# Kernel tuning notes

Hardware: AMD Instinct MI355X
Metric: run time of the kernel (lower is better)

The kernel has to match this reference:

```python
import jax, jax.numpy as jnp
import numpy as np

B, N, DIM = 2, 8192, 3
K = 16            # num_neighbours (dilation=1)
R = 2048          # num_representitives
CIN, CL, COUT = 64, 16, 128
K2 = K * K


def _bn(x, g, b):
    # BatchNorm in eval mode with running_mean=0, running_var=1 -> affine
    return x * g + b


def setup_inputs() -> dict:
    key = jax.random.key(0)
    ks = jax.random.split(key, 24)
    r = lambda i, shape, s=1.0: jax.random.normal(ks[i], shape, jnp.float32) * s
    return {
        "points": r(0, (B, N, DIM)),
        "features": r(1, (B, N, CIN)),
        "lift_w": r(2, (CL, DIM), 0.3), "lift_b": r(3, (CL,), 0.1),
        "bn_lift_g": 1.0 + r(4, (CL,), 0.1), "bn_lift_b": r(5, (CL,), 0.1),
        "t1_w": r(6, (K2, DIM * K), 0.1), "t1_b": r(7, (K2,), 0.1),
        "bn1_g": 1.0 + r(8, (K2,), 0.1), "bn1_b": r(9, (K2,), 0.1),
        "t2_w": r(10, (K2, K2), 0.05), "t2_b": r(11, (K2,), 0.1),
        "bn2_g": 1.0 + r(12, (K2,), 0.1), "bn2_b": r(13, (K2,), 0.1),
        "t3_w": r(14, (K2, K2), 0.05), "t3_b": r(15, (K2,), 0.1),
        "bn3_g": 1.0 + r(16, (K2,), 0.1), "bn3_b": r(17, (K2,), 0.1),
        "conv_w": r(18, (COUT, CIN + CL, K), 0.05), "conv_b": r(19, (COUT,), 0.1),
        "rep_idx": jax.random.permutation(ks[20], N)[:R],
    }


def reference(points, features, lift_w, lift_b, bn_lift_g, bn_lift_b,
              t1_w, t1_b, bn1_g, bn1_b, t2_w, t2_b, bn2_g, bn2_b,
              t3_w, t3_b, bn3_g, bn3_b, conv_w, conv_b, rep_idx):
    b, n, _ = points.shape
    # ---- KNN (squared distance is order-equivalent to torch.cdist) ----
    sq = jnp.sum(points * points, -1)                                   # (b,n)
    d2 = sq[:, :, None] + sq[:, None, :] - 2.0 * jnp.einsum('bnd,bmd->bnm', points, points)
    _, idx = jax.lax.top_k(-d2, K + 1)                                  # (b,n,K+1)
    nn_idx = idx[:, :, 1:]                                              # drop self
    # ---- representative sampling + neighbor gather ----
    rep_pos = points[:, rep_idx]                                        # (b,R,3)
    nb_idx = nn_idx[:, rep_idx]                                         # (b,R,K)
    gather = jax.vmap(lambda arr, i: arr[i])
    nbr_pos = gather(points, nb_idx)                                    # (b,R,K,3)
    nbr_feat = gather(features, nb_idx)                                 # (b,R,K,CIN)
    # ---- X_conv ----
    p = (nbr_pos - rep_pos[:, :, None, :]).reshape(b * R, K, DIM)       # centered
    lifted = jax.nn.relu(_bn(p @ lift_w.T + lift_b, bn_lift_g, bn_lift_b))  # (bR,K,CL)
    feat = jnp.concatenate([lifted, nbr_feat.reshape(b * R, K, CIN)], -1)   # (bR,K,CL+CIN)
    pf = p.reshape(b * R, K * DIM)
    h = jax.nn.relu(_bn(pf @ t1_w.T + t1_b, bn1_g, bn1_b))
    h = jax.nn.relu(_bn(h @ t2_w.T + t2_b, bn2_g, bn2_b))
    T = _bn(h @ t3_w.T + t3_b, bn3_g, bn3_b).reshape(b * R, K, K)       # learned transform
    Tf = jnp.einsum('bij,bjc->bic', T, feat)                            # bmm, (bR,K,C)
    # Conv1d(C, COUT, kernel=K) over length K -> single output position
    out = jnp.einsum('bkc,ock->bo', Tf, conv_w) + conv_b                # (bR,COUT)
    return rep_pos, out.reshape(b, R, COUT)
```

## Files before the change

### kernel.cpp

```cpp
#include <hip/hip_runtime.h>
#include <float.h>

#define Bn 2
#define Nn 8192
#define Rr 2048
#define Kk 16
#define CIN 64
#define CL 16
#define COUT 128
#define K2c 256
#define GT (Bn*Rr)
#define FD (CL+CIN)
#define KC (Kk*FD)
#define MG 4

__global__ __launch_bounds__(256) void prep_kernel(
    const float* __restrict__ t1_w, const float* __restrict__ t2_w,
    const float* __restrict__ t3_w, const float* __restrict__ conv_w,
    const float* __restrict__ points,
    float* __restrict__ t1t, float* __restrict__ t2t,
    float* __restrict__ t3t, float* __restrict__ wp,
    float4* __restrict__ pts4)
{
  int i = blockIdx.x * 256 + threadIdx.x;
  if (i < K2c*48) { int j = i / 48, k = i - j*48; t1t[k*K2c + j] = t1_w[i]; }
  if (i < K2c*K2c) { int j = i >> 8, k = i & 255; t2t[k*K2c + j] = t2_w[i]; t3t[k*K2c + j] = t3_w[i]; }
  if (i < COUT*KC) {
    int o = i / KC, ck = i - o*KC;
    int c = ck >> 4, k = ck & 15;
    wp[(k*FD + c)*COUT + o] = conv_w[i];
  }
  if (i < Bn*Nn) {
    float x = points[i*3+0], y = points[i*3+1], z = points[i*3+2];
    float sq = __fadd_rn(__fadd_rn(__fmul_rn(x,x), __fmul_rn(y,y)), __fmul_rn(z,z));
    pts4[i] = make_float4(x, y, z, sq);
  }
}

__global__ __launch_bounds__(512) void knn_kernel(
    const float4* __restrict__ pts4, const int* __restrict__ rep_idx,
    int* __restrict__ nb_idx, float* __restrict__ p_out,
    float* __restrict__ rep_pos_out)
{
  __shared__ float4 ptsS[3072];
  __shared__ unsigned long long coll[8][128];
  int t    = threadIdx.x;
  int lane = t & 63;
  int w    = t >> 6;
  int g    = blockIdx.x * 8 + w;
  int b    = g >> 11;
  int r    = g & 2047;
  int n    = rep_idx[r];
  const float4* pb4 = pts4 + (size_t)b*Nn;
  float4 Q = pb4[n];
  float qx = Q.x, qy = Q.y, qz = Q.z, sqn = Q.w;

  float c0 = FLT_MAX, c1 = FLT_MAX, c2 = FLT_MAX;
  for (int c = 0; c < 3; c++) {
    int base  = c * 3072;
    int count = (c < 2) ? 3072 : 2048;
    __syncthreads();
    for (int i = t; i < count; i += 512) ptsS[i] = pb4[base + i];
    __syncthreads();
    int iters = count >> 6;
    #pragma unroll 4
    for (int j = 0; j < iters; j++) {
      float4 P = ptsS[j*64 + lane];
      float dot = __fmaf_rn(qz, P.z, __fmaf_rn(qy, P.y, __fmul_rn(qx, P.x)));
      float d2  = __fsub_rn(__fadd_rn(sqn, P.w), __fmul_rn(2.0f, dot));
      float nc2 = __builtin_amdgcn_fmed3f(c1, c2, d2);
      float nc1 = __builtin_amdgcn_fmed3f(c0, c1, d2);
      float nc0 = fminf(c0, d2);
      c0 = nc0; c1 = nc1; c2 = nc2;
    }
  }

  float tau = FLT_MAX;
  for (int rnd = 0; rnd < 6; rnd++) {
    float m = c2;
    #pragma unroll
    for (int off = 1; off < 64; off <<= 1) m = fminf(m, __shfl_xor(m, off));
    if (c2 == m) c2 = FLT_MAX;
    tau = m;
  }

  int cnt = 0;
  #pragma unroll
  for (int cc = 0; cc < 3; cc++) {
    int c = (cc == 0) ? 2 : (cc - 1);
    int base  = c * 3072;
    int count = (c < 2) ? 3072 : 2048;
    if (cc != 0) {
      __syncthreads();
      for (int i = t; i < count; i += 512) ptsS[i] = pb4[base + i];
      __syncthreads();
    }
    int iters = count >> 6;
    #pragma unroll 4
    for (int j = 0; j < iters; j++) {
      float4 P = ptsS[j*64 + lane];
      float dot = __fmaf_rn(qz, P.z, __fmaf_rn(qy, P.y, __fmul_rn(qx, P.x)));
      float d2  = __fsub_rn(__fadd_rn(sqn, P.w), __fmul_rn(2.0f, dot));
      bool pr = (d2 <= tau);
      unsigned long long mask = __ballot(pr);
      if (pr) {
        int pos = cnt + (int)__popcll(mask & ((1ull << lane) - 1ull));
        if (pos < 128) {
          unsigned f = __float_as_uint(d2);
          unsigned mono = f ^ ((unsigned)((int)f >> 31) | 0x80000000u);
          coll[w][pos] = ((unsigned long long)mono << 32) | (unsigned)(base + j*64 + lane);
        }
      }
      cnt += (int)__popcll(mask);
    }
  }
  if (cnt > 128) cnt = 128;

  unsigned long long e1 = (lane < cnt)      ? coll[w][lane]      : ~0ull;
  unsigned long long e2 = (lane + 64 < cnt) ? coll[w][lane + 64] : ~0ull;
  int out_m = 0;
  for (int rnd = 0; rnd < 17; rnd++) {
    unsigned long long myk = (e1 < e2) ? e1 : e2;
    unsigned long long kmin = myk;
    #pragma unroll
    for (int off = 1; off < 64; off <<= 1) {
      unsigned long long o = __shfl_xor(kmin, off);
      kmin = (o < kmin) ? o : kmin;
    }
    if (rnd >= 1 && lane == rnd - 1) out_m = (int)(kmin & 0xFFFFFFFFull);
    if (kmin == e1) e1 = ~0ull;
    else if (kmin == e2) e2 = ~0ull;
  }

  if (lane < 16) {
    nb_idx[g*Kk + lane] = out_m;
    float4 P = pb4[out_m];
    p_out[(g*Kk + lane)*3 + 0] = __fsub_rn(P.x, qx);
    p_out[(g*Kk + lane)*3 + 1] = __fsub_rn(P.y, qy);
    p_out[(g*Kk + lane)*3 + 2] = __fsub_rn(P.z, qz);
  }
  if (lane < 3) rep_pos_out[g*3 + lane] = (lane == 0 ? qx : (lane == 1 ? qy : qz));
}

__device__ __forceinline__ void fma_g(float4& a, float hv, const float4& wv) {
  a.x = fmaf(hv, wv.x, a.x);
  a.y = fmaf(hv, wv.y, a.y);
  a.z = fmaf(hv, wv.z, a.z);
  a.w = fmaf(hv, wv.w, a.w);
}

__global__ __launch_bounds__(256) void mlp_kernel(
    const float* __restrict__ p,
    const float* __restrict__ t1t, const float* __restrict__ t1_b,
    const float* __restrict__ g1v, const float* __restrict__ b1v,
    const float* __restrict__ t2t, const float* __restrict__ t2_b,
    const float* __restrict__ g2v, const float* __restrict__ b2v,
    const float* __restrict__ t3t, const float* __restrict__ t3_b,
    const float* __restrict__ g3v, const float* __restrict__ b3v,
    float* __restrict__ T_out)
{
  __shared__ float pf[48][MG];
  __shared__ float hA[K2c][MG];
  __shared__ float red[4*16*66];
  int t = threadIdx.x;
  int w = t >> 6, l = t & 63;
  int g0 = blockIdx.x * MG;
  for (int e = t; e < MG*48; e += 256) {
    int g = e / 48, k = e - g*48;
    pf[k][g] = p[(size_t)(g0+g)*48 + k];
  }
  __syncthreads();

  float4 acc[MG];

#define LDW(WSRC, K) (*(const float4*)&WSRC[(size_t)(K)*K2c + 4*l])

#define KSTAGE(WSRC, KDIM, HBUF, WB, KK, KNEXT)                        \
  {                                                                    \
    float4 wc = WB;                                                    \
    if ((KNEXT) < KDIM) WB = LDW(WSRC, KNEXT);                         \
    float4 h = *(const float4*)&HBUF[KK][0];                           \
    fma_g(acc[0], h.x, wc); fma_g(acc[1], h.y, wc);                    \
    fma_g(acc[2], h.z, wc); fma_g(acc[3], h.w, wc);                    \
  }

#define KLOOP(WSRC, KDIM, HBUF)                                        \
  {                                                                    \
    _Pragma("unroll")                                                  \
    for (int q = 0; q < MG; q++) acc[q] = make_float4(0.f,0.f,0.f,0.f);\
    float4 wb0 = LDW(WSRC, w);                                         \
    float4 wb1 = (w + 4  < KDIM) ? LDW(WSRC, w + 4)  : wb0;            \
    float4 wb2 = (w + 8  < KDIM) ? LDW(WSRC, w + 8)  : wb0;            \
    float4 wb3 = (w + 12 < KDIM) ? LDW(WSRC, w + 12) : wb0;            \
    for (int k = w; k < KDIM; k += 16) {                               \
      KSTAGE(WSRC, KDIM, HBUF, wb0, k,      k + 16)                    \
      if (k + 4 < KDIM)  KSTAGE(WSRC, KDIM, HBUF, wb1, k + 4,  k + 20) \
      if (k + 8 < KDIM)  KSTAGE(WSRC, KDIM, HBUF, wb2, k + 8,  k + 24) \
      if (k + 12 < KDIM) KSTAGE(WSRC, KDIM, HBUF, wb3, k + 12, k + 28) \
    }                                                                  \
  }

#define WRITE_RED()                                                    \
  {                                                                    \
    _Pragma("unroll")                                                  \
    for (int q = 0; q < MG; q++) {                                     \
      red[(w*16 + 0*4 + q)*66 + l] = acc[q].x;                         \
      red[(w*16 + 1*4 + q)*66 + l] = acc[q].y;                         \
      red[(w*16 + 2*4 + q)*66 + l] = acc[q].z;                         \
      red[(w*16 + 3*4 + q)*66 + l] = acc[q].w;                         \
    }                                                                  \
  }

#define REDUCE(S)                                                      \
  float4 S = make_float4(0.f,0.f,0.f,0.f);                             \
  {                                                                    \
    int lr = t >> 2, cc = t & 3;                                       \
    _Pragma("unroll")                                                  \
    for (int ww = 0; ww < 4; ww++) {                                   \
      S.x += red[(ww*16 + cc*4 + 0)*66 + lr];                          \
      S.y += red[(ww*16 + cc*4 + 1)*66 + lr];                          \
      S.z += red[(ww*16 + cc*4 + 2)*66 + lr];                          \
      S.w += red[(ww*16 + cc*4 + 3)*66 + lr];                          \
    }                                                                  \
  }

  KLOOP(t1t, 48, pf)
  WRITE_RED()
  __syncthreads();
  {
    REDUCE(s)
    float bb = t1_b[t], gg = g1v[t], oo = b1v[t];
    float4 v;
    v.x = fmaxf(fmaf(s.x + bb, gg, oo), 0.f);
    v.y = fmaxf(fmaf(s.y + bb, gg, oo), 0.f);
    v.z = fmaxf(fmaf(s.z + bb, gg, oo), 0.f);
    v.w = fmaxf(fmaf(s.w + bb, gg, oo), 0.f);
    *(float4*)&hA[t][0] = v;
  }
  __syncthreads();

  KLOOP(t2t, K2c, hA)
  WRITE_RED()
  __syncthreads();
  {
    REDUCE(s)
    float bb = t2_b[t], gg = g2v[t], oo = b2v[t];
    float4 v;
    v.x = fmaxf(fmaf(s.x + bb, gg, oo), 0.f);
    v.y = fmaxf(fmaf(s.y + bb, gg, oo), 0.f);
    v.z = fmaxf(fmaf(s.z + bb, gg, oo), 0.f);
    v.w = fmaxf(fmaf(s.w + bb, gg, oo), 0.f);
    *(float4*)&hA[t][0] = v;
  }
  __syncthreads();

  KLOOP(t3t, K2c, hA)
  WRITE_RED()
  __syncthreads();
  {
    REDUCE(s)
    float bb = t3_b[t], gg = g3v[t], oo = b3v[t];
    T_out[(size_t)(g0+0)*K2c + t] = fmaf(s.x + bb, gg, oo);
    T_out[(size_t)(g0+1)*K2c + t] = fmaf(s.y + bb, gg, oo);
    T_out[(size_t)(g0+2)*K2c + t] = fmaf(s.z + bb, gg, oo);
    T_out[(size_t)(g0+3)*K2c + t] = fmaf(s.w + bb, gg, oo);
  }
#undef KLOOP
#undef KSTAGE
#undef LDW
#undef WRITE_RED
#undef REDUCE
}

__global__ __launch_bounds__(256) void tf_kernel(
    const float* __restrict__ T_in, const float* __restrict__ features,
    const float* __restrict__ p, const int* __restrict__ nb_idx,
    const float* __restrict__ lift_w, const float* __restrict__ lift_b,
    const float* __restrict__ bng, const float* __restrict__ bnb,
    float* __restrict__ Tf)
{
  __shared__ float T_s[4*K2c];
  __shared__ float f_s[4*KC];
  __shared__ float ps[4*48];
  __shared__ int   idxs[64];
  __shared__ float lw[48], lb2[16], lg[16], lo[16];
  int t = threadIdx.x;
  int g0 = blockIdx.x * 4;
  int b = g0 / Rr;
  for (int e = t; e < 4*K2c; e += 256) T_s[e] = T_in[(size_t)g0*K2c + e];
  if (t >= 32 && t < 224) {
    int e = t - 32;
    ps[e] = p[(size_t)g0*48 + e];
  }
  if (t < 64) idxs[t] = nb_idx[g0*16 + t];
  if (t >= 64 && t < 112)  lw[t-64]   = lift_w[t-64];
  if (t >= 112 && t < 128) lb2[t-112] = lift_b[t-112];
  if (t >= 224 && t < 240) lg[t-224]  = bng[t-224];
  if (t >= 240)            lo[t-240]  = bnb[t-240];
  __syncthreads();

  {
    int wv = t >> 6, ln = t & 63;
    for (int row = wv; row < 64; row += 4) {
      int gg = row >> 4, k = row & 15;
      f_s[gg*KC + k*FD + CL + ln] = features[((size_t)b*Nn + idxs[row])*CIN + ln];
    }
  }
  for (int e = t; e < 1024; e += 256) {
    int gg = e >> 8, rem = e & 255, k = rem >> 4, c = rem & 15;
    float acc = ps[gg*48 + k*3 + 0]*lw[c*3+0] + ps[gg*48 + k*3 + 1]*lw[c*3+1]
              + ps[gg*48 + k*3 + 2]*lw[c*3+2] + lb2[c];
    acc = acc*lg[c] + lo[c];
    f_s[gg*KC + k*FD + c] = fmaxf(acc, 0.f);
  }
  __syncthreads();

  int gg = t >> 6;
  int cl = t & 63;
  for (int ci = cl; ci < FD; ci += 64) {
    float fcol[16];
    #pragma unroll
    for (int j = 0; j < 16; j++) fcol[j] = f_s[gg*KC + j*FD + ci];
    #pragma unroll
    for (int k = 0; k < 16; k++) {
      float acc = 0.f;
      #pragma unroll
      for (int j = 0; j < 16; j++) acc = fmaf(T_s[gg*K2c + k*16 + j], fcol[j], acc);
      Tf[(size_t)(g0+gg)*KC + k*FD + ci] = acc;
    }
  }
}

__global__ __launch_bounds__(256) void gemm_kernel(
    const float* __restrict__ A,
    const float* __restrict__ Bm,
    float* __restrict__ part)
{
  __shared__ float As[16*36];
  __shared__ float Bs[16*COUT];
  int t = threadIdx.x;
  int m0 = blockIdx.x * 32;
  int ky = blockIdx.y;
  int kbase0 = ky * (KC/8);
  float acc[4][4];
  #pragma unroll
  for (int i = 0; i < 4; i++)
    #pragma unroll
    for (int j = 0; j < 4; j++) acc[i][j] = 0.f;
  int tn = t & 31, tm = t >> 5;

  for (int kt = 0; kt < KC/8; kt += 16) {
    int kb = kbase0 + kt;
    {
      int kcol = t & 15, row = t >> 4;
      As[kcol*36 + row]      = A[(size_t)(m0+row)*KC + kb + kcol];
      As[kcol*36 + row + 16] = A[(size_t)(m0+row+16)*KC + kb + kcol];
    }
    {
      int o = t & 127, kk2 = t >> 7;
      #pragma unroll
      for (int p4 = 0; p4 < 8; p4++) {
        int kk = kk2 + p4*2;
        Bs[kk*COUT + o] = Bm[(size_t)(kb+kk)*COUT + o];
      }
    }
    __syncthreads();
    #pragma unroll
    for (int kk = 0; kk < 16; kk++) {
      float4 a4 = *(const float4*)&As[kk*36 + tm*4];
      float4 b4 = *(const float4*)&Bs[kk*COUT + tn*4];
      float av[4] = {a4.x, a4.y, a4.z, a4.w};
      float bv[4] = {b4.x, b4.y, b4.z, b4.w};
      #pragma unroll
      for (int i = 0; i < 4; i++)
        #pragma unroll
        for (int j = 0; j < 4; j++) acc[i][j] = fmaf(av[i], bv[j], acc[i][j]);
    }
    __syncthreads();
  }
  #pragma unroll
  for (int i = 0; i < 4; i++) {
    float4 v = make_float4(acc[i][0], acc[i][1], acc[i][2], acc[i][3]);
    *(float4*)&part[((size_t)ky*GT + m0 + tm*4 + i)*COUT + tn*4] = v;
  }
}

__global__ __launch_bounds__(256) void reduce_kernel(
    const float* __restrict__ part, const float* __restrict__ conv_b,
    float* __restrict__ outp)
{
  int i = blockIdx.x*256 + threadIdx.x;
  float4 s = ((const float4*)conv_b)[i & 31];
  #pragma unroll
  for (int w = 0; w < 8; w++) {
    float4 v = ((const float4*)(part + (size_t)w*GT*COUT))[i];
    s.x += v.x; s.y += v.y; s.z += v.z; s.w += v.w;
  }
  ((float4*)outp)[i] = s;
}

extern "C" void kernel_launch(void* const* d_in, const int* in_sizes, int n_in,
                              void* d_out, int out_size, void* d_ws, size_t ws_size,
                              hipStream_t stream) {
  const float* points   = (const float*)d_in[0];
  const float* features = (const float*)d_in[1];
  const float* lift_w   = (const float*)d_in[2];
  const float* lift_b   = (const float*)d_in[3];
  const float* bn_lift_g= (const float*)d_in[4];
  const float* bn_lift_b= (const float*)d_in[5];
  const float* t1_w     = (const float*)d_in[6];
  const float* t1_b     = (const float*)d_in[7];
  const float* bn1_g    = (const float*)d_in[8];
  const float* bn1_b    = (const float*)d_in[9];
  const float* t2_w     = (const float*)d_in[10];
  const float* t2_b     = (const float*)d_in[11];
  const float* bn2_g    = (const float*)d_in[12];
  const float* bn2_b    = (const float*)d_in[13];
  const float* t3_w     = (const float*)d_in[14];
  const float* t3_b     = (const float*)d_in[15];
  const float* bn3_g    = (const float*)d_in[16];
  const float* bn3_b    = (const float*)d_in[17];
  const float* conv_w   = (const float*)d_in[18];
  const float* conv_b   = (const float*)d_in[19];
  const int*   rep_idx  = (const int*)d_in[20];

  char* ws = (char*)d_ws;
  int*    nb   = (int*)   (ws + 0);
  float*  p    = (float*) (ws + 262144);
  float*  T    = (float*) (ws + 1048576);
  float*  Tf   = (float*) (ws + 5242880);
  float*  wp   = (float*) (ws + 26214400);
  float*  t1t  = (float*) (ws + 26869760);
  float*  t2t  = (float*) (ws + 26918912);
  float*  t3t  = (float*) (ws + 27181056);
  float*  part = (float*) (ws + 33554432);
  float4* pts4 = (float4*)(ws + 52428800);

  float* rep_pos = (float*)d_out;
  float* outp    = (float*)d_out + (size_t)GT*3;

  prep_kernel<<<640, 256, 0, stream>>>(t1_w, t2_w, t3_w, conv_w, points,
                                       t1t, t2t, t3t, wp, pts4);
  knn_kernel<<<GT/8, 512, 0, stream>>>(pts4, rep_idx, nb, p, rep_pos);
  mlp_kernel<<<GT/MG, 256, 0, stream>>>(p, t1t, t1_b, bn1_g, bn1_b,
                                        t2t, t2_b, bn2_g, bn2_b,
                                        t3t, t3_b, bn3_g, bn3_b, T);
  tf_kernel<<<GT/4, 256, 0, stream>>>(T, features, p, nb,
                                      lift_w, lift_b, bn_lift_g, bn_lift_b, Tf);
  dim3 ggrid(GT/32, 8);
  gemm_kernel<<<ggrid, 256, 0, stream>>>(Tf, wp, part);
  reduce_kernel<<<(GT*COUT/4)/256, 256, 0, stream>>>(part, conv_b, outp);
}
```

Measured before the change: 220.1 us.

## Process two queries per wave in KNN and fuse MLP with transform kernel

The KNN kernel now has each wavefront handle two representative queries, so every point loaded from shared memory serves two distance computations and the grid is halved. The MLP kernel and the feature-transform kernel are merged, so the learned 16x16 transform stays in shared memory and is no longer written to and re-read from global memory. The costs are more registers and shared memory per block, which can lower occupancy, and only 256 KNN blocks, which may underfill the GPU.

Result: slower. 277.5 us (+26.0%).

```diff
diff --git a/kernel.cpp b/kernel.cpp
--- a/kernel.cpp
+++ b/kernel.cpp
@@ -43,19 +43,21 @@
     float* __restrict__ rep_pos_out)
 {
   __shared__ float4 ptsS[3072];
-  __shared__ unsigned long long coll[8][128];
+  __shared__ unsigned long long coll[8][2][128];
   int t    = threadIdx.x;
   int lane = t & 63;
   int w    = t >> 6;
-  int g    = blockIdx.x * 8 + w;
-  int b    = g >> 11;
-  int r    = g & 2047;
-  int n    = rep_idx[r];
+  int gA   = blockIdx.x * 16 + w*2;
+  int b    = gA >> 11;
+  int rA   = gA & 2047;
+  int nA   = rep_idx[rA];
+  int nB   = rep_idx[rA + 1];
   const float4* pb4 = pts4 + (size_t)b*Nn;
-  float4 Q = pb4[n];
-  float qx = Q.x, qy = Q.y, qz = Q.z, sqn = Q.w;
-
-  float c0 = FLT_MAX, c1 = FLT_MAX, c2 = FLT_MAX;
+  float4 QA = pb4[nA];
+  float4 QB = pb4[nB];
+
+  float a0 = FLT_MAX, a1 = FLT_MAX, a2 = FLT_MAX;
+  float b0 = FLT_MAX, b1 = FLT_MAX, b2 = FLT_MAX;
   for (int c = 0; c < 3; c++) {
     int base  = c * 3072;
     int count = (c < 2) ? 3072 : 2048;
@@ -66,25 +68,38 @@
     #pragma unroll 4
     for (int j = 0; j < iters; j++) {
       float4 P = ptsS[j*64 + lane];
-      float dot = __fmaf_rn(qz, P.z, __fmaf_rn(qy, P.y, __fmul_rn(qx, P.x)));
-      float d2  = __fsub_rn(__fadd_rn(sqn, P.w), __fmul_rn(2.0f, dot));
-      float nc2 = __builtin_amdgcn_fmed3f(c1, c2, d2);
-      float nc1 = __builtin_amdgcn_fmed3f(c0, c1, d2);
-      float nc0 = fminf(c0, d2);
-      c0 = nc0; c1 = nc1; c2 = nc2;
-    }
-  }
-
-  float tau = FLT_MAX;
+      float dotA = __fmaf_rn(QA.z, P.z, __fmaf_rn(QA.y, P.y, __fmul_rn(QA.x, P.x)));
+      float d2A  = __fsub_rn(__fadd_rn(QA.w, P.w), __fmul_rn(2.0f, dotA));
+      float dotB = __fmaf_rn(QB.z, P.z, __fmaf_rn(QB.y, P.y, __fmul_rn(QB.x, P.x)));
+      float d2B  = __fsub_rn(__fadd_rn(QB.w, P.w), __fmul_rn(2.0f, dotB));
+      float na2 = __builtin_amdgcn_fmed3f(a1, a2, d2A);
+      float na1 = __builtin_amdgcn_fmed3f(a0, a1, d2A);
+      float na0 = fminf(a0, d2A);
+      a0 = na0; a1 = na1; a2 = na2;
+      float nb2 = __builtin_amdgcn_fmed3f(b1, b2, d2B);
+      float nb1 = __builtin_amdgcn_fmed3f(b0, b1, d2B);
+      float nb0 = fminf(b0, d2B);
+      b0 = nb0; b1 = nb1; b2 = nb2;
+    }
+  }
+
+  float tauA = FLT_MAX, tauB = FLT_MAX;
   for (int rnd = 0; rnd < 6; rnd++) {
-    float m = c2;
+    float m = a2;
     #pragma unroll
     for (int off = 1; off < 64; off <<= 1) m = fminf(m, __shfl_xor(m, off));
-    if (c2 == m) c2 = FLT_MAX;
-    tau = m;
-  }
-
-  int cnt = 0;
+    if (a2 == m) a2 = FLT_MAX;
+    tauA = m;
+  }
+  for (int rnd = 0; rnd < 6; rnd++) {
+    float m = b2;
+    #pragma unroll
+    for (int off = 1; off < 64; off <<= 1) m = fminf(m, __shfl_xor(m, off));
+    if (b2 == m) b2 = FLT_MAX;
+    tauB = m;
+  }
+
+  int cntA = 0, cntB = 0;
   #pragma unroll
   for (int cc = 0; cc < 3; cc++) {
     int c = (cc == 0) ? 2 : (cc - 1);
@@ -99,47 +114,69 @@
     #pragma unroll 4
     for (int j = 0; j < iters; j++) {
       float4 P = ptsS[j*64 + lane];
-      float dot = __fmaf_rn(qz, P.z, __fmaf_rn(qy, P.y, __fmul_rn(qx, P.x)));
-      float d2  = __fsub_rn(__fadd_rn(sqn, P.w), __fmul_rn(2.0f, dot));
-      bool pr = (d2 <= tau);
-      unsigned long long mask = __ballot(pr);
-      if (pr) {
-        int pos = cnt + (int)__popcll(mask & ((1ull << lane) - 1ull));
+      int m = base + j*64 + lane;
+      float dotA = __fmaf_rn(QA.z, P.z, __fmaf_rn(QA.y, P.y, __fmul_rn(QA.x, P.x)));
+      float d2A  = __fsub_rn(__fadd_rn(QA.w, P.w), __fmul_rn(2.0f, dotA));
+      bool prA = (d2A <= tauA);
+      unsigned long long maskA = __ballot(prA);
+      if (prA) {
+        int pos = cntA + (int)__popcll(maskA & ((1ull << lane) - 1ull));
         if (pos < 128) {
-          unsigned f = __float_as_uint(d2);
+          unsigned f = __float_as_uint(d2A);
           unsigned mono = f ^ ((unsigned)((int)f >> 31) | 0x80000000u);
-          coll[w][pos] = ((unsigned long long)mono << 32) | (unsigned)(base + j*64 + lane);
+          coll[w][0][pos] = ((unsigned long long)mono << 32) | (unsigned)m;
         }
       }
-      cnt += (int)__popcll(mask);
-    }
-  }
-  if (cnt > 128) cnt = 128;
-
-  unsigned long long e1 = (lane < cnt)      ? coll[w][lane]      : ~0ull;
-  unsigned long long e2 = (lane + 64 < cnt) ? coll[w][lane + 64] : ~0ull;
-  int out_m = 0;
-  for (int rnd = 0; rnd < 17; rnd++) {
-    unsigned long long myk = (e1 < e2) ? e1 : e2;
-    unsigned long long kmin = myk;
-    #pragma unroll
-    for (int off = 1; off < 64; off <<= 1) {
-      unsigned long long o = __shfl_xor(kmin, off);
-      kmin = (o < kmin) ? o : kmin;
-    }
-    if (rnd >= 1 && lane == rnd - 1) out_m = (int)(kmin & 0xFFFFFFFFull);
-    if (kmin == e1) e1 = ~0ull;
-    else if (kmin == e2) e2 = ~0ull;
-  }
-
-  if (lane < 16) {
-    nb_idx[g*Kk + lane] = out_m;
-    float4 P = pb4[out_m];
-    p_out[(g*Kk + lane)*3 + 0] = __fsub_rn(P.x, qx);
-    p_out[(g*Kk + lane)*3 + 1] = __fsub_rn(P.y, qy);
-    p_out[(g*Kk + lane)*3 + 2] = __fsub_rn(P.z, qz);
-  }
-  if (lane < 3) rep_pos_out[g*3 + lane] = (lane == 0 ? qx : (lane == 1 ? qy : qz));
+      cntA += (int)__popcll(maskA);
+      float dotB = __fmaf_rn(QB.z, P.z, __fmaf_rn(QB.y, P.y, __fmul_rn(QB.x, P.x)));
+      float d2B  = __fsub_rn(__fadd_rn(QB.w, P.w), __fmul_rn(2.0f, dotB));
+      bool prB = (d2B <= tauB);
+      unsigned long long maskB = __ballot(prB);
+      if (prB) {
+        int pos = cntB + (int)__popcll(maskB & ((1ull << lane) - 1ull));
+        if (pos < 128) {
+          unsigned f = __float_as_uint(d2B);
+          unsigned mono = f ^ ((unsigned)((int)f >> 31) | 0x80000000u);
+          coll[w][1][pos] = ((unsigned long long)mono << 32) | (unsigned)m;
+        }
+      }
+      cntB += (int)__popcll(maskB);
+    }
+  }
+  if (cntA > 128) cntA = 128;
+  if (cntB > 128) cntB = 128;
+
+  #pragma unroll
+  for (int q = 0; q < 2; q++) {
+    int cnt = q ? cntB : cntA;
+    int g   = gA + q;
+    float qx = q ? QB.x : QA.x;
+    float qy = q ? QB.y : QA.y;
+    float qz = q ? QB.z : QA.z;
+    unsigned long long e1 = (lane < cnt)      ? coll[w][q][lane]      : ~0ull;
+    unsigned long long e2 = (lane + 64 < cnt) ? coll[w][q][lane + 64] : ~0ull;
+    int out_m = 0;
+    for (int rnd = 0; rnd < 17; rnd++) {
+      unsigned long long myk = (e1 < e2) ? e1 : e2;
+      unsigned long long kmin = myk;
+      #pragma unroll
+      for (int off = 1; off < 64; off <<= 1) {
+        unsigned long long o = __shfl_xor(kmin, off);
+        kmin = (o < kmin) ? o : kmin;
+      }
+      if (rnd >= 1 && lane == rnd - 1) out_m = (int)(kmin & 0xFFFFFFFFull);
+      if (kmin == e1) e1 = ~0ull;
+      else if (kmin == e2) e2 = ~0ull;
+    }
+    if (lane < 16) {
+      nb_idx[g*Kk + lane] = out_m;
+      float4 P = pb4[out_m];
+      p_out[(g*Kk + lane)*3 + 0] = __fsub_rn(P.x, qx);
+      p_out[(g*Kk + lane)*3 + 1] = __fsub_rn(P.y, qy);
+      p_out[(g*Kk + lane)*3 + 2] = __fsub_rn(P.z, qz);
+    }
+    if (lane < 3) rep_pos_out[g*3 + lane] = (lane == 0 ? qx : (lane == 1 ? qy : qz));
+  }
 }
 
 __device__ __forceinline__ void fma_g(float4& a, float hv, const float4& wv) {
@@ -149,7 +186,7 @@
   a.w = fmaf(hv, wv.w, a.w);
 }
 
-__global__ __launch_bounds__(256) void mlp_kernel(
+__global__ __launch_bounds__(256) void mlptf_kernel(
     const float* __restrict__ p,
     const float* __restrict__ t1t, const float* __restrict__ t1_b,
     const float* __restrict__ g1v, const float* __restrict__ b1v,
@@ -157,18 +194,32 @@
     const float* __restrict__ g2v, const float* __restrict__ b2v,
     const float* __restrict__ t3t, const float* __restrict__ t3_b,
     const float* __restrict__ g3v, const float* __restrict__ b3v,
-    float* __restrict__ T_out)
+    const float* __restrict__ features, const int* __restrict__ nb_idx,
+    const float* __restrict__ lift_w, const float* __restrict__ lift_b,
+    const float* __restrict__ bng, const float* __restrict__ bnb,
+    float* __restrict__ Tf)
 {
   __shared__ float pf[48][MG];
   __shared__ float hA[K2c][MG];
-  __shared__ float red[4*16*66];
+  __shared__ float T_s[MG*K2c];
+  __shared__ float uni[MG*KC];
+  __shared__ float ps[MG*48];
+  __shared__ int   idxs[64];
+  __shared__ float lw[48], lb2[16], lg[16], lo[16];
   int t = threadIdx.x;
   int w = t >> 6, l = t & 63;
   int g0 = blockIdx.x * MG;
+  int b = g0 / Rr;
   for (int e = t; e < MG*48; e += 256) {
     int g = e / 48, k = e - g*48;
     pf[k][g] = p[(size_t)(g0+g)*48 + k];
-  }
+    ps[e]    = p[(size_t)g0*48 + e];
+  }
+  if (t < 64) idxs[t] = nb_idx[g0*16 + t];
+  if (t >= 64 && t < 112)  lw[t-64]   = lift_w[t-64];
+  if (t >= 112 && t < 128) lb2[t-112] = lift_b[t-112];
+  if (t >= 128 && t < 144) lg[t-128]  = bng[t-128];
+  if (t >= 144 && t < 160) lo[t-144]  = bnb[t-144];
   __syncthreads();
 
   float4 acc[MG];
@@ -204,10 +255,10 @@
   {                                                                    \
     _Pragma("unroll")                                                  \
     for (int q = 0; q < MG; q++) {                                     \
-      red[(w*16 + 0*4 + q)*66 + l] = acc[q].x;                         \
-      red[(w*16 + 1*4 + q)*66 + l] = acc[q].y;                         \
-      red[(w*16 + 2*4 + q)*66 + l] = acc[q].z;                         \
-      red[(w*16 + 3*4 + q)*66 + l] = acc[q].w;                         \
+      uni[(w*16 + 0*4 + q)*66 + l] = acc[q].x;                         \
+      uni[(w*16 + 1*4 + q)*66 + l] = acc[q].y;                         \
+      uni[(w*16 + 2*4 + q)*66 + l] = acc[q].z;                         \
+      uni[(w*16 + 3*4 + q)*66 + l] = acc[q].w;                         \
     }                                                                  \
   }
 
@@ -217,10 +268,10 @@
     int lr = t >> 2, cc = t & 3;                                       \
     _Pragma("unroll")                                                  \
     for (int ww = 0; ww < 4; ww++) {                                   \
-      S.x += red[(ww*16 + cc*4 + 0)*66 + lr];                          \
-      S.y += red[(ww*16 + cc*4 + 1)*66 + lr];                          \
-      S.z += red[(ww*16 + cc*4 + 2)*66 + lr];                          \
-      S.w += red[(ww*16 + cc*4 + 3)*66 + lr];                          \
+      S.x += uni[(ww*16 + cc*4 + 0)*66 + lr];                          \
+      S.y += uni[(ww*16 + cc*4 + 1)*66 + lr];                          \
+      S.z += uni[(ww*16 + cc*4 + 2)*66 + lr];                          \
+      S.w += uni[(ww*16 + cc*4 + 3)*66 + lr];                          \
     }                                                                  \
   }
 
@@ -260,75 +311,50 @@
   {
     REDUCE(s)
     float bb = t3_b[t], gg = g3v[t], oo = b3v[t];
-    T_out[(size_t)(g0+0)*K2c + t] = fmaf(s.x + bb, gg, oo);
-    T_out[(size_t)(g0+1)*K2c + t] = fmaf(s.y + bb, gg, oo);
-    T_out[(size_t)(g0+2)*K2c + t] = fmaf(s.z + bb, gg, oo);
-    T_out[(size_t)(g0+3)*K2c + t] = fmaf(s.w + bb, gg, oo);
+    T_s[0*K2c + t] = fmaf(s.x + bb, gg, oo);
+    T_s[1*K2c + t] = fmaf(s.y + bb, gg, oo);
+    T_s[2*K2c + t] = fmaf(s.z + bb, gg, oo);
+    T_s[3*K2c + t] = fmaf(s.w + bb, gg, oo);
+  }
+  __syncthreads();
+
+  {
+    int wv = t >> 6, ln = t & 63;
+    for (int row = wv; row < 64; row += 4) {
+      int gg = row >> 4, k = row & 15;
+      uni[gg*KC + k*FD + CL + ln] = features[((size_t)b*Nn + idxs[row])*CIN + ln];
+    }
+  }
+  for (int e = t; e < 1024; e += 256) {
+    int gg = e >> 8, rem = e & 255, k = rem >> 4, c = rem & 15;
+    float acc1 = ps[gg*48 + k*3 + 0]*lw[c*3+0] + ps[gg*48 + k*3 + 1]*lw[c*3+1]
+               + ps[gg*48 + k*3 + 2]*lw[c*3+2] + lb2[c];
+    acc1 = acc1*lg[c] + lo[c];
+    uni[gg*KC + k*FD + c] = fmaxf(acc1, 0.f);
+  }
+  __syncthreads();
+
+  {
+    int gg = t >> 6;
+    int cl = t & 63;
+    for (int ci = cl; ci < FD; ci += 64) {
+      float fcol[16];
+      #pragma unroll
+      for (int j = 0; j < 16; j++) fcol[j] = uni[gg*KC + j*FD + ci];
+      #pragma unroll
+      for (int k = 0; k < 16; k++) {
+        float a1 = 0.f;
+        #pragma unroll
+        for (int j = 0; j < 16; j++) a1 = fmaf(T_s[gg*K2c + k*16 + j], fcol[j], a1);
+        Tf[(size_t)(g0+gg)*KC + k*FD + ci] = a1;
+      }
+    }
   }
 #undef KLOOP
 #undef KSTAGE
 #undef LDW
 #undef WRITE_RED
 #undef REDUCE
-}
-
-__global__ __launch_bounds__(256) void tf_kernel(
-    const float* __restrict__ T_in, const float* __restrict__ features,
-    const float* __restrict__ p, const int* __restrict__ nb_idx,
-    const float* __restrict__ lift_w, const float* __restrict__ lift_b,
-    const float* __restrict__ bng, const float* __restrict__ bnb,
-    float* __restrict__ Tf)
-{
-  __shared__ float T_s[4*K2c];
-  __shared__ float f_s[4*KC];
-  __shared__ float ps[4*48];
-  __shared__ int   idxs[64];
-  __shared__ float lw[48], lb2[16], lg[16], lo[16];
-  int t = threadIdx.x;
-  int g0 = blockIdx.x * 4;
-  int b = g0 / Rr;
-  for (int e = t; e < 4*K2c; e += 256) T_s[e] = T_in[(size_t)g0*K2c + e];
-  if (t >= 32 && t < 224) {
-    int e = t - 32;
-    ps[e] = p[(size_t)g0*48 + e];
-  }
-  if (t < 64) idxs[t] = nb_idx[g0*16 + t];
-  if (t >= 64 && t < 112)  lw[t-64]   = lift_w[t-64];
-  if (t >= 112 && t < 128) lb2[t-112] = lift_b[t-112];
-  if (t >= 224 && t < 240) lg[t-224]  = bng[t-224];
-  if (t >= 240)            lo[t-240]  = bnb[t-240];
-  __syncthreads();
-
-  {
-    int wv = t >> 6, ln = t & 63;
-    for (int row = wv; row < 64; row += 4) {
-      int gg = row >> 4, k = row & 15;
-      f_s[gg*KC + k*FD + CL + ln] = features[((size_t)b*Nn + idxs[row])*CIN + ln];
-    }
-  }
-  for (int e = t; e < 1024; e += 256) {
-    int gg = e >> 8, rem = e & 255, k = rem >> 4, c = rem & 15;
-    float acc = ps[gg*48 + k*3 + 0]*lw[c*3+0] + ps[gg*48 + k*3 + 1]*lw[c*3+1]
-              + ps[gg*48 + k*3 + 2]*lw[c*3+2] + lb2[c];
-    acc = acc*lg[c] + lo[c];
-    f_s[gg*KC + k*FD + c] = fmaxf(acc, 0.f);
-  }
-  __syncthreads();
-
-  int gg = t >> 6;
-  int cl = t & 63;
-  for (int ci = cl; ci < FD; ci += 64) {
-    float fcol[16];
-    #pragma unroll
-    for (int j = 0; j < 16; j++) fcol[j] = f_s[gg*KC + j*FD + ci];
-    #pragma unroll
-    for (int k = 0; k < 16; k++) {
-      float acc = 0.f;
-      #pragma unroll
-      for (int j = 0; j < 16; j++) acc = fmaf(T_s[gg*K2c + k*16 + j], fcol[j], acc);
-      Tf[(size_t)(g0+gg)*KC + k*FD + ci] = acc;
-    }
-  }
 }
 
 __global__ __launch_bounds__(256) void gemm_kernel(
@@ -427,7 +453,6 @@
   char* ws = (char*)d_ws;
   int*    nb   = (int*)   (ws + 0);
   float*  p    = (float*) (ws + 262144);
-  float*  T    = (float*) (ws + 1048576);
   float*  Tf   = (float*) (ws + 5242880);
   float*  wp   = (float*) (ws + 26214400);
   float*  t1t  = (float*) (ws + 26869760);
@@ -441,12 +466,13 @@
 
   prep_kernel<<<640, 256, 0, stream>>>(t1_w, t2_w, t3_w, conv_w, points,
                                        t1t, t2t, t3t, wp, pts4);
-  knn_kernel<<<GT/8, 512, 0, stream>>>(pts4, rep_idx, nb, p, rep_pos);
-  mlp_kernel<<<GT/MG, 256, 0, stream>>>(p, t1t, t1_b, bn1_g, bn1_b,
-                                        t2t, t2_b, bn2_g, bn2_b,
-                                        t3t, t3_b, bn3_g, bn3_b, T);
-  tf_kernel<<<GT/4, 256, 0, stream>>>(T, features, p, nb,
-                                      lift_w, lift_b, bn_lift_g, bn_lift_b, Tf);
+  knn_kernel<<<GT/16, 512, 0, stream>>>(pts4, rep_idx, nb, p, rep_pos);
+  mlptf_kernel<<<GT/MG, 256, 0, stream>>>(p, t1t, t1_b, bn1_g, bn1_b,
+                                          t2t, t2_b, bn2_g, bn2_b,
+                                          t3t, t3_b, bn3_g, bn3_b,
+                                          features, nb,
+                                          lift_w, lift_b, bn_lift_g, bn_lift_b,
+                                          Tf);
   dim3 ggrid(GT/32, 8);
   gemm_kernel<<<ggrid, 256, 0, stream>>>(Tf, wp, part);
   reduce_kernel<<<(GT*COUT/4)/256, 256, 0, stream>>>(part, conv_b, outp);
```
